# Kernel optimization log

Hardware: AMD Instinct MI355X
Metric: run time of the kernel (lower is better)

## Reference

```python
import jax, jax.numpy as jnp
import numpy as np
import math

B, S, D, H = 8, 1024, 768, 12
DEPTH = D // H
MAX_LEN = 1024


def setup_inputs() -> dict:
    key = jax.random.key(0)
    ks = jax.random.split(key, 16)
    inp = {
        "Q": jax.random.normal(ks[0], (B, S, D), dtype=jnp.float32),
        "K": jax.random.normal(ks[1], (B, S, D), dtype=jnp.float32),
        "V": jax.random.normal(ks[2], (B, S, D), dtype=jnp.float32),
        # additive mask: 1 where attention is disallowed (causal upper triangle)
        "mask": jnp.triu(jnp.ones((S, S), dtype=jnp.float32), k=1)[None, None],
        "Wq": jax.random.normal(ks[3], (D, D), dtype=jnp.float32) / math.sqrt(D),
        "bq": jnp.zeros((D,), dtype=jnp.float32),
        "Wk": jax.random.normal(ks[4], (D, D), dtype=jnp.float32) / math.sqrt(D),
        "bk": jnp.zeros((D,), dtype=jnp.float32),
        "Wv": jax.random.normal(ks[5], (D, D), dtype=jnp.float32) / math.sqrt(D),
        "bv": jnp.zeros((D,), dtype=jnp.float32),
        "Wo": jax.random.normal(ks[6], (D, D), dtype=jnp.float32) / math.sqrt(D),
        "bo": jnp.zeros((D,), dtype=jnp.float32),
        "Er": jax.random.normal(ks[7], (MAX_LEN, DEPTH), dtype=jnp.float32),
    }
    return inp


def _skew(QEr):
    # QEr: [B,H,S,S] -> pad one zero col on the left, reshape, drop first row
    b, h, s, _ = QEr.shape
    padded = jnp.pad(QEr, ((0, 0), (0, 0), (0, 0), (1, 0)))  # [B,H,S,S+1]
    reshaped = padded.reshape(b, h, s + 1, s)
    return reshaped[:, :, 1:, :]  # [B,H,S,S]


def reference(Q, K, V, mask, Wq, bq, Wk, bk, Wv, bv, Wo, bo, Er):
    batch, seq, d_model = Q.shape
    q = (Q @ Wq.T + bq).reshape(batch, seq, H, DEPTH).transpose(0, 2, 1, 3)
    k = (K @ Wk.T + bk).reshape(batch, seq, H, DEPTH).transpose(0, 2, 1, 3)
    v = (V @ Wv.T + bv).reshape(batch, seq, H, DEPTH).transpose(0, 2, 1, 3)

    # relative position bias via skew trick
    QEr = jnp.einsum('bhsd,td->bhst', q, Er[:seq])
    Srel = _skew(QEr)

    logits = (jnp.einsum('bhsd,bhtd->bhst', q, k) + Srel) / math.sqrt(DEPTH)
    logits = logits + mask * (-1e9)
    attn = jax.nn.softmax(logits, axis=-1)  # [B,H,S,S]
    out = jnp.einsum('bhst,bhtd->bhsd', attn, v)
    out = out.transpose(0, 2, 1, 3).reshape(batch, seq, d_model)
    out = out @ Wo.T + bo
    return out
```

## Files before the change

### kernel.cpp

```cpp
#include <hip/hip_runtime.h>

typedef __bf16 bf16_t;
typedef __bf16 bf16x8 __attribute__((ext_vector_type(8)));
typedef float  f32x4  __attribute__((ext_vector_type(4)));

#define MFMA16(a, b, c) __builtin_amdgcn_mfma_f32_16x16x32_bf16((a), (b), (c), 0, 0, 0)
#define LOG2E 1.44269504f

#define DPP_ROR(x, N) __int_as_float(__builtin_amdgcn_update_dpp( \
    0, __float_as_int(x), 0x120 + (N), 0xF, 0xF, true))

__device__ inline bf16x8 load8(const bf16_t* p) { return *(const bf16x8*)p; }
__device__ inline bf16x8 load8(const float* p) {
    f32x4 a = *(const f32x4*)p;
    f32x4 b = *(const f32x4*)(p + 4);
    bf16x8 r;
    r[0] = (bf16_t)a[0]; r[1] = (bf16_t)a[1]; r[2] = (bf16_t)a[2]; r[3] = (bf16_t)a[3];
    r[4] = (bf16_t)b[0]; r[5] = (bf16_t)b[1]; r[6] = (bf16_t)b[2]; r[7] = (bf16_t)b[3];
    return r;
}

__global__ void __launch_bounds__(256)
cvt_all(const float* __restrict__ Q, const float* __restrict__ K,
        const float* __restrict__ V, const float* __restrict__ Wq,
        const float* __restrict__ Wk, const float* __restrict__ Wv,
        const float* __restrict__ Wo, const float* __restrict__ Er,
        bf16_t* __restrict__ qxb, bf16_t* __restrict__ kxb,
        bf16_t* __restrict__ vxb, bf16_t* __restrict__ wqb,
        bf16_t* __restrict__ wkb, bf16_t* __restrict__ wvb,
        bf16_t* __restrict__ wob, bf16_t* __restrict__ Erb)
{
    const int idx = blockIdx.x * 256 + threadIdx.x;
    const float* src;  bf16_t* dst;  int off;
    if      (idx <  786432) { src = Q;  dst = qxb; off = idx; }
    else if (idx < 1572864) { src = K;  dst = kxb; off = idx -  786432; }
    else if (idx < 2359296) { src = V;  dst = vxb; off = idx - 1572864; }
    else if (idx < 2433024) { src = Wq; dst = wqb; off = idx - 2359296; }
    else if (idx < 2506752) { src = Wk; dst = wkb; off = idx - 2433024; }
    else if (idx < 2580480) { src = Wv; dst = wvb; off = idx - 2506752; }
    else if (idx < 2654208) { src = Wo; dst = wob; off = idx - 2580480; }
    else {
        off = idx - 2654208;
        bf16x8 r;
        if (off < 8192) r = load8(Er + (size_t)off * 8);
        else { for (int j = 0; j < 8; ++j) r[j] = (bf16_t)0.0f; }
        *(bf16x8*)(Erb + (size_t)off * 8) = r;
        return;
    }
    *(bf16x8*)(dst + (size_t)off * 8) = load8(src + (size_t)off * 8);
}

template <typename OT>
__device__ __forceinline__ void
gemm_bt(const bf16_t* __restrict__ X, const bf16_t* __restrict__ W,
        const float* __restrict__ bias, OT* __restrict__ Out, int mode,
        int m0, int n0, bf16_t* Al, bf16_t* Bl)
{
    const int tid  = threadIdx.x;
    const int w    = tid >> 6;
    const int lane = tid & 63;
    const int quad = lane >> 4;
    const int l16  = lane & 15;
    const int wr   = (w >> 1) * 64;
    const int wc   = (w & 1) * 64;
    const int l8r  = lane >> 3;
    const int l8c  = lane & 7;

    f32x4 acc[4][4];
#pragma unroll
    for (int mi = 0; mi < 4; ++mi)
#pragma unroll
        for (int ni = 0; ni < 4; ++ni)
#pragma unroll
            for (int r = 0; r < 4; ++r) acc[mi][ni][r] = 0.0f;

    const bf16_t* gA = X + (size_t)(m0 + w * 32 + l8r) * 768 + l8c * 8;
    const bf16_t* gB = W + (size_t)(n0 + w * 32 + l8r) * 768 + l8c * 8;

    for (int kc = 0; kc < 12; ++kc) {
        const int k0 = kc * 64;
        __syncthreads();
#pragma unroll
        for (int p = 0; p < 4; ++p) {
            __builtin_amdgcn_global_load_lds(
                (__attribute__((address_space(1))) const void*)(gA + (size_t)p * 8 * 768 + k0),
                (__attribute__((address_space(3))) void*)(Al + (w * 4 + p) * 528), 16, 0, 0);
            __builtin_amdgcn_global_load_lds(
                (__attribute__((address_space(1))) const void*)(gB + (size_t)p * 8 * 768 + k0),
                (__attribute__((address_space(3))) void*)(Bl + (w * 4 + p) * 528), 16, 0, 0);
        }
        __syncthreads();
#pragma unroll
        for (int kk = 0; kk < 2; ++kk) {
            bf16x8 a[4], b[4];
#pragma unroll
            for (int mi = 0; mi < 4; ++mi) {
                const int row = wr + mi * 16 + l16;
                a[mi] = *(const bf16x8*)&Al[(row >> 3) * 528 + (row & 7) * 64 + kk * 32 + quad * 8];
            }
#pragma unroll
            for (int ni = 0; ni < 4; ++ni) {
                const int row = wc + ni * 16 + l16;
                b[ni] = *(const bf16x8*)&Bl[(row >> 3) * 528 + (row & 7) * 64 + kk * 32 + quad * 8];
            }
#pragma unroll
            for (int mi = 0; mi < 4; ++mi)
#pragma unroll
                for (int ni = 0; ni < 4; ++ni)
                    acc[mi][ni] = MFMA16(a[mi], b[ni], acc[mi][ni]);
        }
    }

#pragma unroll
    for (int ni = 0; ni < 4; ++ni) {
        const int n  = n0 + wc + ni * 16 + l16;
        const float bn = bias[n];
#pragma unroll
        for (int mi = 0; mi < 4; ++mi) {
#pragma unroll
            for (int r = 0; r < 4; ++r) {
                const int m = m0 + wr + mi * 16 + quad * 4 + r;
                const float v = acc[mi][ni][r] + bn;
                if (mode == 0) {
                    const int bb = m >> 10, ss = m & 1023, hh = n >> 6, dd = n & 63;
                    Out[(((size_t)(bb * 12 + hh)) * 1024 + ss) * 64 + dd] = (OT)v;
                } else if (mode == 2) {
                    const int bb = m >> 10, ss = m & 1023, hh = n >> 6, dd = n & 63;
                    Out[(((size_t)(bb * 12 + hh)) * 64 + dd) * 1024 + ss] = (OT)v;
                } else {
                    Out[(size_t)m * 768 + n] = (OT)v;
                }
            }
        }
    }
}

__global__ void __launch_bounds__(256)
qkv_proj(const bf16_t* __restrict__ Qx, const bf16_t* __restrict__ Kx,
         const bf16_t* __restrict__ Vx,
         const bf16_t* __restrict__ Wq, const bf16_t* __restrict__ Wk,
         const bf16_t* __restrict__ Wv,
         const float* __restrict__ bq, const float* __restrict__ bk,
         const float* __restrict__ bv,
         bf16_t* __restrict__ qo, bf16_t* __restrict__ ko, bf16_t* __restrict__ vo)
{
    __shared__ bf16_t Al[16 * 528];
    __shared__ bf16_t Bl[16 * 528];
    const int z = blockIdx.z;
    const bf16_t* X  = (z == 0) ? Qx : (z == 1) ? Kx : Vx;
    const bf16_t* W  = (z == 0) ? Wq : (z == 1) ? Wk : Wv;
    const float* bs  = (z == 0) ? bq : (z == 1) ? bk : bv;
    bf16_t* Out      = (z == 0) ? qo : (z == 1) ? ko : vo;
    gemm_bt<bf16_t>(X, W, bs, Out, (z == 2) ? 2 : 0,
                    blockIdx.x * 128, blockIdx.y * 128, Al, Bl);
}

__global__ void __launch_bounds__(256)
out_proj(const bf16_t* __restrict__ X, const bf16_t* __restrict__ W,
         const float* __restrict__ bias, float* __restrict__ Out)
{
    __shared__ bf16_t Al[16 * 528];
    __shared__ bf16_t Bl[16 * 528];
    gemm_bt<float>(X, W, bias, Out, 1, blockIdx.x * 128, blockIdx.y * 128, Al, Bl);
}

__global__ void __launch_bounds__(256)
attn_kernel(const bf16_t* __restrict__ qb, const bf16_t* __restrict__ kb,
            const bf16_t* __restrict__ vt, const bf16_t* __restrict__ Erb,
            bf16_t* __restrict__ att)
{
    __shared__ bf16_t Kl[64][72];
    __shared__ bf16_t Vtl[64][72];
    __shared__ bf16_t Erl[128][72];
    __shared__ bf16_t Pl[4][16][72];

    const int tid  = threadIdx.x;
    const int bid  = blockIdx.x;
    const int bh   = bid >> 3;
    const int pr   = bid & 7;
    const int b    = bh / 12;
    const int h    = bh % 12;
    const int w    = tid >> 6;
    const int lane = tid & 63;
    const int quad = lane >> 4;
    const int l16  = lane & 15;
    const int u0   = 48 - 16 * w;
    const int srow = tid >> 3;
    const int scol = (tid & 7) * 8;

    const bf16_t* qp = qb + (size_t)bh * 65536;
    const bf16_t* kp = kb + (size_t)bh * 65536;
    const bf16_t* vp = vt + (size_t)bh * 65536;

#pragma unroll 1
    for (int phase = 0; phase < 2; ++phase) {
        const int qt  = phase ? (15 - pr) : pr;
        const int s0  = qt * 64;
        const int s0w = s0 + 16 * w;
        const int E00 = 960 - s0;

        bf16x8 aq[2];
#pragma unroll
        for (int kk = 0; kk < 2; ++kk)
            aq[kk] = load8(qp + (size_t)(s0w + l16) * 64 + kk * 32 + quad * 8);

        __syncthreads();

#pragma unroll
        for (int p = 0; p < 2; ++p) {
            *(bf16x8*)&Kl[p * 32 + srow][scol]  = load8(kp + (size_t)(p * 32 + srow) * 64 + scol);
            *(bf16x8*)&Vtl[p * 32 + srow][scol] = load8(vp + (size_t)(p * 32 + srow) * 1024 + scol);
        }
#pragma unroll
        for (int p = 0; p < 4; ++p) {
            const int e = E00 + p * 32 + srow;
            *(bf16x8*)&Erl[e & 127][scol] = load8(Erb + (size_t)e * 64 + scol);
        }
        __syncthreads();

        float mrow[4], lrow[4];
        f32x4 o[4];
#pragma unroll
        for (int r = 0; r < 4; ++r) { mrow[r] = -1e30f; lrow[r] = 0.0f; }
#pragma unroll
        for (int nt = 0; nt < 4; ++nt)
#pragma unroll
            for (int r = 0; r < 4; ++r) o[nt][r] = 0.0f;

        const int nT = qt + 1;
        for (int tt = 0; tt < nT; ++tt) {
            const int t0 = tt * 64;
            const int E0 = E00 + t0;
            const bool more = (tt + 1 < nT);

            bf16x8 kpre[2], vpre[2], epre[2];
            if (more) {
                const int t0n = t0 + 64;
#pragma unroll
                for (int p = 0; p < 2; ++p) {
                    kpre[p] = load8(kp + (size_t)(t0n + p * 32 + srow) * 64 + scol);
                    vpre[p] = load8(vp + (size_t)(p * 32 + srow) * 1024 + t0n + scol);
                    const int e = E0 + 128 + p * 32 + srow;
                    epre[p] = load8(Erb + (size_t)e * 64 + scol);
                }
            }

            f32x4 sacc[4], gacc[5];
#pragma unroll
            for (int nt = 0; nt < 4; ++nt)
#pragma unroll
                for (int r = 0; r < 4; ++r) sacc[nt][r] = 0.0f;
#pragma unroll
            for (int gt = 0; gt < 5; ++gt)
#pragma unroll
                for (int r = 0; r < 4; ++r) gacc[gt][r] = 0.0f;

            __builtin_amdgcn_s_setprio(1);
#pragma unroll
            for (int kk = 0; kk < 2; ++kk) {
#pragma unroll
                for (int nt = 0; nt < 4; ++nt) {
                    if (t0 + nt * 16 <= s0w + 15) {
                        bf16x8 bk_ = *(const bf16x8*)&Kl[nt * 16 + l16][kk * 32 + quad * 8];
                        sacc[nt] = MFMA16(aq[kk], bk_, sacc[nt]);
                    }
                }
#pragma unroll
                for (int gt = 0; gt < 5; ++gt) {
                    const int er = (E0 + u0 + gt * 16 + l16) & 127;
                    bf16x8 be = *(const bf16x8*)&Erl[er][kk * 32 + quad * 8];
                    gacc[gt] = MFMA16(aq[kk], be, gacc[gt]);
                }
            }
            __builtin_amdgcn_s_setprio(0);

#pragma unroll
            for (int r = 0; r < 4; ++r) {
                const int i   = quad * 4 + r;
                const int cc  = 15 - i + l16;
                const int src = (lane & 48) | (cc & 15);
                const bool lo = (cc < 16);
                float rot[5];
#pragma unroll
                for (int gt = 0; gt < 5; ++gt) rot[gt] = __shfl(gacc[gt][r], src);
#pragma unroll
                for (int nt = 0; nt < 4; ++nt) {
                    const float g = lo ? rot[nt] : rot[nt + 1];
                    float sv = (sacc[nt][r] + g) * 0.125f;
                    if (t0 + nt * 16 + l16 > s0w + i) sv = -1e9f;
                    sacc[nt][r] = sv;
                }
            }

#pragma unroll
            for (int r = 0; r < 4; ++r) {
                float vm = fmaxf(fmaxf(sacc[0][r], sacc[1][r]), fmaxf(sacc[2][r], sacc[3][r]));
                vm = fmaxf(vm, DPP_ROR(vm, 8));
                vm = fmaxf(vm, DPP_ROR(vm, 4));
                vm = fmaxf(vm, DPP_ROR(vm, 2));
                vm = fmaxf(vm, DPP_ROR(vm, 1));
                const float mnew  = fmaxf(mrow[r], vm);
                const float alpha = __builtin_exp2f((mrow[r] - mnew) * LOG2E);
                mrow[r] = mnew;
                float rs = 0.0f;
#pragma unroll
                for (int nt = 0; nt < 4; ++nt) {
                    const float p_ = __builtin_exp2f((sacc[nt][r] - mnew) * LOG2E);
                    sacc[nt][r] = p_;
                    rs += p_;
                }
                rs += DPP_ROR(rs, 8);
                rs += DPP_ROR(rs, 4);
                rs += DPP_ROR(rs, 2);
                rs += DPP_ROR(rs, 1);
                lrow[r] = lrow[r] * alpha + rs;
                o[0][r] *= alpha; o[1][r] *= alpha;
                o[2][r] *= alpha; o[3][r] *= alpha;
            }

#pragma unroll
            for (int nt = 0; nt < 4; ++nt)
#pragma unroll
                for (int r = 0; r < 4; ++r)
                    Pl[w][quad * 4 + r][nt * 16 + l16] = (bf16_t)sacc[nt][r];

            __builtin_amdgcn_s_setprio(1);
#pragma unroll
            for (int kk = 0; kk < 2; ++kk) {
                bf16x8 ap = *(const bf16x8*)&Pl[w][l16][kk * 32 + quad * 8];
#pragma unroll
                for (int nt = 0; nt < 4; ++nt) {
                    bf16x8 bv_ = *(const bf16x8*)&Vtl[nt * 16 + l16][kk * 32 + quad * 8];
                    o[nt] = MFMA16(ap, bv_, o[nt]);
                }
            }
            __builtin_amdgcn_s_setprio(0);

            if (more) {
                __syncthreads();
#pragma unroll
                for (int p = 0; p < 2; ++p) {
                    *(bf16x8*)&Kl[p * 32 + srow][scol]  = kpre[p];
                    *(bf16x8*)&Vtl[p * 32 + srow][scol] = vpre[p];
                    const int e = E0 + p * 32 + srow;
                    *(bf16x8*)&Erl[e & 127][scol] = epre[p];
                }
                __syncthreads();
            }
        }

#pragma unroll
        for (int nt = 0; nt < 4; ++nt) {
#pragma unroll
            for (int r = 0; r < 4; ++r) {
                const int s_idx = s0w + quad * 4 + r;
                const int d     = nt * 16 + l16;
                att[((size_t)b * 1024 + s_idx) * 768 + h * 64 + d] = (bf16_t)(o[nt][r] / lrow[r]);
            }
        }
    }
}

extern "C" void kernel_launch(void* const* d_in, const int* in_sizes, int n_in,
                              void* d_out, int out_size, void* d_ws, size_t ws_size,
                              hipStream_t stream)
{
    const float* Q  = (const float*)d_in[0];
    const float* K  = (const float*)d_in[1];
    const float* V  = (const float*)d_in[2];
    const float* Wq = (const float*)d_in[4];
    const float* bq = (const float*)d_in[5];
    const float* Wk = (const float*)d_in[6];
    const float* bk = (const float*)d_in[7];
    const float* Wv = (const float*)d_in[8];
    const float* bv = (const float*)d_in[9];
    const float* Wo = (const float*)d_in[10];
    const float* bo = (const float*)d_in[11];
    const float* Er = (const float*)d_in[12];
    float* out      = (float*)d_out;

    const size_t per = (size_t)8 * 12 * 1024 * 64;
    const size_t wsz = (size_t)768 * 768;

    bf16_t* qxb   = (bf16_t*)d_out;
    bf16_t* qbuf  = qxb + per;

    bf16_t* kbuf  = (bf16_t*)d_ws;
    bf16_t* vtbuf = kbuf + per;
    bf16_t* kxb   = vtbuf + per;
    bf16_t* vxb   = kxb + per;
    bf16_t* wqb   = vxb + per;
    bf16_t* wkb   = wqb + wsz;
    bf16_t* wvb   = wkb + wsz;
    bf16_t* wob   = wvb + wsz;
    bf16_t* Erb   = wob + wsz;
    bf16_t* abuf  = kxb;

    cvt_all<<<dim3(10404), dim3(256), 0, stream>>>(Q, K, V, Wq, Wk, Wv, Wo, Er,
                                                   qxb, kxb, vxb, wqb, wkb, wvb,
                                                   wob, Erb);
    qkv_proj<<<dim3(64, 6, 3), dim3(256), 0, stream>>>(qxb, kxb, vxb, wqb, wkb, wvb,
                                                       bq, bk, bv, qbuf, kbuf, vtbuf);
    attn_kernel<<<dim3(768), dim3(256), 0, stream>>>(qbuf, kbuf, vtbuf, Erb, abuf);
    out_proj<<<dim3(64, 6), dim3(256), 0, stream>>>(abuf, wob, bo, out);
}
```

Before: 308.9 us.

## Fold softmax scale into Q projection, seed QK accumulator with rel-pos bias, lazy rescale

```diff
diff --git a/kernel.cpp b/kernel.cpp
--- a/kernel.cpp
+++ b/kernel.cpp
@@ -54,7 +54,7 @@
 __device__ __forceinline__ void
 gemm_bt(const bf16_t* __restrict__ X, const bf16_t* __restrict__ W,
         const float* __restrict__ bias, OT* __restrict__ Out, int mode,
-        int m0, int n0, bf16_t* Al, bf16_t* Bl)
+        float oscale, int m0, int n0, bf16_t* Al, bf16_t* Bl)
 {
     const int tid  = threadIdx.x;
     const int w    = tid >> 6;
@@ -120,7 +120,7 @@
 #pragma unroll
             for (int r = 0; r < 4; ++r) {
                 const int m = m0 + wr + mi * 16 + quad * 4 + r;
-                const float v = acc[mi][ni][r] + bn;
+                const float v = (acc[mi][ni][r] + bn) * oscale;
                 if (mode == 0) {
                     const int bb = m >> 10, ss = m & 1023, hh = n >> 6, dd = n & 63;
                     Out[(((size_t)(bb * 12 + hh)) * 1024 + ss) * 64 + dd] = (OT)v;
@@ -152,6 +152,7 @@
     const float* bs  = (z == 0) ? bq : (z == 1) ? bk : bv;
     bf16_t* Out      = (z == 0) ? qo : (z == 1) ? ko : vo;
     gemm_bt<bf16_t>(X, W, bs, Out, (z == 2) ? 2 : 0,
+                    (z == 0) ? 0.125f : 1.0f,
                     blockIdx.x * 128, blockIdx.y * 128, Al, Bl);
 }
 
@@ -161,7 +162,7 @@
 {
     __shared__ bf16_t Al[16 * 528];
     __shared__ bf16_t Bl[16 * 528];
-    gemm_bt<float>(X, W, bias, Out, 1, blockIdx.x * 128, blockIdx.y * 128, Al, Bl);
+    gemm_bt<float>(X, W, bias, Out, 1, 1.0f, blockIdx.x * 128, blockIdx.y * 128, Al, Bl);
 }
 
 __global__ void __launch_bounds__(256)
@@ -247,10 +248,6 @@
 
             f32x4 sacc[4], gacc[5];
 #pragma unroll
-            for (int nt = 0; nt < 4; ++nt)
-#pragma unroll
-                for (int r = 0; r < 4; ++r) sacc[nt][r] = 0.0f;
-#pragma unroll
             for (int gt = 0; gt < 5; ++gt)
 #pragma unroll
                 for (int r = 0; r < 4; ++r) gacc[gt][r] = 0.0f;
@@ -258,13 +255,6 @@
             __builtin_amdgcn_s_setprio(1);
 #pragma unroll
             for (int kk = 0; kk < 2; ++kk) {
-#pragma unroll
-                for (int nt = 0; nt < 4; ++nt) {
-                    if (t0 + nt * 16 <= s0w + 15) {
-                        bf16x8 bk_ = *(const bf16x8*)&Kl[nt * 16 + l16][kk * 32 + quad * 8];
-                        sacc[nt] = MFMA16(aq[kk], bk_, sacc[nt]);
-                    }
-                }
 #pragma unroll
                 for (int gt = 0; gt < 5; ++gt) {
                     const int er = (E0 + u0 + gt * 16 + l16) & 127;
@@ -284,38 +274,85 @@
 #pragma unroll
                 for (int gt = 0; gt < 5; ++gt) rot[gt] = __shfl(gacc[gt][r], src);
 #pragma unroll
+                for (int nt = 0; nt < 4; ++nt)
+                    sacc[nt][r] = lo ? rot[nt] : rot[nt + 1];
+            }
+
+            __builtin_amdgcn_s_setprio(1);
+#pragma unroll
+            for (int kk = 0; kk < 2; ++kk) {
+#pragma unroll
                 for (int nt = 0; nt < 4; ++nt) {
-                    const float g = lo ? rot[nt] : rot[nt + 1];
-                    float sv = (sacc[nt][r] + g) * 0.125f;
-                    if (t0 + nt * 16 + l16 > s0w + i) sv = -1e9f;
-                    sacc[nt][r] = sv;
-                }
-            }
-
+                    if (t0 + nt * 16 <= s0w + 15) {
+                        bf16x8 bk_ = *(const bf16x8*)&Kl[nt * 16 + l16][kk * 32 + quad * 8];
+                        sacc[nt] = MFMA16(aq[kk], bk_, sacc[nt]);
+                    }
+                }
+            }
+            __builtin_amdgcn_s_setprio(0);
+
+#pragma unroll
+            for (int nt = 0; nt < 4; ++nt) {
+                if (t0 + nt * 16 + 15 > s0w) {
+#pragma unroll
+                    for (int r = 0; r < 4; ++r) {
+                        const int i = quad * 4 + r;
+                        if (t0 + nt * 16 + l16 > s0w + i) sacc[nt][r] = -1e9f;
+                    }
+                }
+            }
+
+            float vm[4];
 #pragma unroll
             for (int r = 0; r < 4; ++r) {
-                float vm = fmaxf(fmaxf(sacc[0][r], sacc[1][r]), fmaxf(sacc[2][r], sacc[3][r]));
-                vm = fmaxf(vm, DPP_ROR(vm, 8));
-                vm = fmaxf(vm, DPP_ROR(vm, 4));
-                vm = fmaxf(vm, DPP_ROR(vm, 2));
-                vm = fmaxf(vm, DPP_ROR(vm, 1));
-                const float mnew  = fmaxf(mrow[r], vm);
-                const float alpha = __builtin_exp2f((mrow[r] - mnew) * LOG2E);
-                mrow[r] = mnew;
-                float rs = 0.0f;
-#pragma unroll
-                for (int nt = 0; nt < 4; ++nt) {
-                    const float p_ = __builtin_exp2f((sacc[nt][r] - mnew) * LOG2E);
-                    sacc[nt][r] = p_;
-                    rs += p_;
-                }
-                rs += DPP_ROR(rs, 8);
-                rs += DPP_ROR(rs, 4);
-                rs += DPP_ROR(rs, 2);
-                rs += DPP_ROR(rs, 1);
-                lrow[r] = lrow[r] * alpha + rs;
-                o[0][r] *= alpha; o[1][r] *= alpha;
-                o[2][r] *= alpha; o[3][r] *= alpha;
+                float v_ = fmaxf(fmaxf(sacc[0][r], sacc[1][r]), fmaxf(sacc[2][r], sacc[3][r]));
+                v_ = fmaxf(v_, DPP_ROR(v_, 8));
+                v_ = fmaxf(v_, DPP_ROR(v_, 4));
+                v_ = fmaxf(v_, DPP_ROR(v_, 2));
+                v_ = fmaxf(v_, DPP_ROR(v_, 1));
+                vm[r] = v_;
+            }
+            const bool nogrow = (vm[0] <= mrow[0] + 8.0f) && (vm[1] <= mrow[1] + 8.0f) &&
+                                (vm[2] <= mrow[2] + 8.0f) && (vm[3] <= mrow[3] + 8.0f);
+            if (__all(nogrow)) {
+#pragma unroll
+                for (int r = 0; r < 4; ++r) {
+                    const float mL = mrow[r] * LOG2E;
+                    float rs = 0.0f;
+#pragma unroll
+                    for (int nt = 0; nt < 4; ++nt) {
+                        const float p_ = __builtin_exp2f(__builtin_fmaf(sacc[nt][r], LOG2E, -mL));
+                        sacc[nt][r] = p_;
+                        rs += p_;
+                    }
+                    rs += DPP_ROR(rs, 8);
+                    rs += DPP_ROR(rs, 4);
+                    rs += DPP_ROR(rs, 2);
+                    rs += DPP_ROR(rs, 1);
+                    lrow[r] += rs;
+                }
+            } else {
+#pragma unroll
+                for (int r = 0; r < 4; ++r) {
+                    const float mnew = fmaxf(mrow[r], vm[r]);
+                    const float mL   = mnew * LOG2E;
+                    const float alpha = __builtin_exp2f(__builtin_fmaf(mrow[r], LOG2E, -mL));
+                    mrow[r] = mnew;
+                    float rs = 0.0f;
+#pragma unroll
+                    for (int nt = 0; nt < 4; ++nt) {
+                        const float p_ = __builtin_exp2f(__builtin_fmaf(sacc[nt][r], LOG2E, -mL));
+                        sacc[nt][r] = p_;
+                        rs += p_;
+                    }
+                    rs += DPP_ROR(rs, 8);
+                    rs += DPP_ROR(rs, 4);
+                    rs += DPP_ROR(rs, 2);
+                    rs += DPP_ROR(rs, 1);
+                    lrow[r] = lrow[r] * alpha + rs;
+                    o[0][r] *= alpha; o[1][r] *= alpha;
+                    o[2][r] *= alpha; o[3][r] *= alpha;
+                }
             }
 
 #pragma unroll
```

New measurement: 322.4 us. +4.4%, slower.
